# Kernel tuning notes

Hardware: AMD Instinct MI355X
Metric: run time of the kernel (lower is better)

Reference implementation:

```python
import jax, jax.numpy as jnp
import numpy as np

B, C_IN, N = 16, 64, 40962          # icosphere level-6 node count
C_OUT = 32                           # out_feats; conv emits 7*C_OUT channels
NEW_N = 4 * N - 6                    # 163842
SEVEN_N = 7 * N                      # gather domain after reshape


def setup_inputs() -> dict:
    key = jax.random.key(0)
    k1, k2, k3, k4, k5 = jax.random.split(key, 5)
    x = jax.random.normal(k1, (B, C_IN, N), dtype=jnp.float32)
    W = jax.random.normal(k2, (7 * C_OUT, C_IN), dtype=jnp.float32) * (1.0 / np.sqrt(C_IN))
    b = jax.random.normal(k3, (7 * C_OUT,), dtype=jnp.float32) * 0.01
    top_idx = jax.random.randint(k4, (N,), 0, SEVEN_N, dtype=jnp.int64 if jax.config.jax_enable_x64 else jnp.int32)
    down_idx = jax.random.randint(k5, ((3 * N - 6) * 2,), 0, SEVEN_N, dtype=jnp.int64 if jax.config.jax_enable_x64 else jnp.int32)
    return {"x": x, "W": W, "b": b, "top_idx": top_idx, "down_idx": down_idx}


def reference(x, W, b, top_idx, down_idx):
    Bsz, _, n = x.shape
    c_out = W.shape[0] // 7
    # pointwise (kernel_size=1) Conv1d == GEMM over channels: [B,7*out,N]
    y = jnp.einsum('bcn,oc->bon', x, W) + b[None, :, None]
    # torch .view(B, out, 7N): row-major reshape, identical in jax
    y = y.reshape(Bsz, c_out, 7 * n)
    x1 = y[:, :, top_idx]                               # [B, out, N]
    x2 = y[:, :, down_idx].reshape(Bsz, c_out, -1, 2)   # [B, out, 3N-6, 2]
    out = jnp.concatenate([x1, x2.mean(axis=3)], axis=2)  # [B, out, 4N-6]
    return out
```

## Files before the change

### kernel.cpp

```cpp
#include <hip/hip_runtime.h>
#include <hip/hip_fp16.h>

#define BB     16
#define CIN    64
#define NN     40962
#define COUT   32
#define NEWN   (4*NN - 6)
#define GROUPS_PER_B ((NEWN + 31)/32)
#define NGROUPS (BB * GROUPS_PER_B)

typedef _Float16 f16x8  __attribute__((ext_vector_type(8)));
typedef float    f32x16 __attribute__((ext_vector_type(16)));
typedef _Float16 h2     __attribute__((ext_vector_type(2)));

__device__ __forceinline__ int pk_add_h2(int a, int b) {
  h2 r = __builtin_bit_cast(h2, a) + __builtin_bit_cast(h2, b);
  return __builtin_bit_cast(int, r);
}
__device__ __forceinline__ int pack2(float lo, float hi) {
  h2 r; r.x = (_Float16)lo; r.y = (_Float16)hi;
  return __builtin_bit_cast(int, r);
}

__global__ __launch_bounds__(256) void k_transpose(const float* __restrict__ x,
                                                   __half* __restrict__ xT) {
  __shared__ float tile[64][65];
  const int b  = blockIdx.y;
  const int n0 = blockIdx.x * 64;
  const int lx = threadIdx.x & 63;
  const int ly = threadIdx.x >> 6;
  const float* xb = x + (size_t)b * CIN * NN;
  const int n = n0 + lx;
#pragma unroll
  for (int i = 0; i < 16; ++i) {
    int c = i * 4 + ly;
    tile[c][lx] = (n < NN) ? xb[(size_t)c * NN + n] : 0.f;
  }
  __syncthreads();
  __half* xTb = xT + (size_t)b * NN * CIN;
#pragma unroll
  for (int i = 0; i < 16; ++i) {
    int nl = i * 4 + ly;
    int nn = n0 + nl;
    if (nn < NN) xTb[(size_t)nn * CIN + lx] = __float2half(tile[lx][nl]);
  }
}

__global__ __launch_bounds__(256, 2) void k_upconv_mfma(
    const __half* __restrict__ xT, const float* __restrict__ W,
    const float* __restrict__ bias, const int* __restrict__ top,
    const int* __restrict__ down, float* __restrict__ out) {
  const int lane = threadIdx.x & 63;
  const int co   = lane & 31;
  const int h    = lane >> 5;
  const int waveInBlock = threadIdx.x >> 6;
  const int gwave = blockIdx.x * (blockDim.x >> 6) + waveInBlock;
  const int nwaves = gridDim.x * (blockDim.x >> 6);

  int4 Af[29];
#pragma unroll
  for (int s = 0; s < 28; ++s) {
    const int t  = s >> 2;
    const int c0 = 16 * (s & 3) + 8 * h;
    const float* wr = W + (co * 7 + t) * 64 + c0;
    float4 wa = *(const float4*)wr;
    float4 wb = *(const float4*)(wr + 4);
    Af[s].x = pack2(0.5f * wa.x, 0.5f * wa.y);
    Af[s].y = pack2(0.5f * wa.z, 0.5f * wa.w);
    Af[s].z = pack2(0.5f * wb.x, 0.5f * wb.y);
    Af[s].w = pack2(0.5f * wb.z, 0.5f * wb.w);
  }
  {
    int4 ab = {0, 0, 0, 0};
    if (h == 0) {
      float bv[8];
#pragma unroll
      for (int tau = 0; tau < 7; ++tau) bv[tau] = 0.5f * bias[co * 7 + tau];
      bv[7] = 0.f;
      ab.x = pack2(bv[0], bv[1]);
      ab.y = pack2(bv[2], bv[3]);
      ab.z = pack2(bv[4], bv[5]);
      ab.w = pack2(bv[6], bv[7]);
    }
    Af[28] = ab;
  }

  for (int gid = gwave; gid < NGROUPS; gid += nwaves) {
    const int b = gid / GROUPS_PER_B;
    const int g = gid - b * GROUPS_PER_B;
    const int k = g * 32 + co;
    const bool valid = (k < NEWN);

    int j1 = 0, j2 = 0;
    if (valid) {
      if (k < NN) { j1 = top[k]; j2 = j1; }
      else {
        const int kk = k - NN;
        j1 = down[2 * kk];
        j2 = down[2 * kk + 1];
      }
    }
    const int t0 = j1 / NN, n0 = j1 - t0 * NN;
    const int t1 = j2 / NN, n1 = j2 - t1 * NN;

    const __half* xTb = xT + (size_t)b * NN * CIN;
    const int4* base0 = (const int4*)(xTb + (size_t)n0 * CIN);
    const int4* base1 = (const int4*)(xTb + (size_t)n1 * CIN);
    int4 col0[4], col1[4];
#pragma unroll
    for (int q = 0; q < 4; ++q) col0[q] = base0[2 * q + h];
#pragma unroll
    for (int q = 0; q < 4; ++q) col1[q] = base1[2 * q + h];

    f32x16 acc;
#pragma unroll
    for (int i = 0; i < 16; ++i) acc[i] = 0.f;

#pragma unroll
    for (int s = 0; s < 28; ++s) {
      const int t = s >> 2, q = s & 3;
      const bool m0 = (t0 == t), m1 = (t1 == t);
      int4 bb;
      bb.x = pk_add_h2(m0 ? col0[q].x : 0, m1 ? col1[q].x : 0);
      bb.y = pk_add_h2(m0 ? col0[q].y : 0, m1 ? col1[q].y : 0);
      bb.z = pk_add_h2(m0 ? col0[q].z : 0, m1 ? col1[q].z : 0);
      bb.w = pk_add_h2(m0 ? col0[q].w : 0, m1 ? col1[q].w : 0);
      acc = __builtin_amdgcn_mfma_f32_32x32x16_f16(
          __builtin_bit_cast(f16x8, Af[s]), __builtin_bit_cast(f16x8, bb), acc, 0, 0, 0);
    }

    {
      int4 bsel = {0, 0, 0, 0};
      if (h == 0) {
        float c0f = (float)((t0 == 0) + (t1 == 0));
        float c1f = (float)((t0 == 1) + (t1 == 1));
        float c2f = (float)((t0 == 2) + (t1 == 2));
        float c3f = (float)((t0 == 3) + (t1 == 3));
        float c4f = (float)((t0 == 4) + (t1 == 4));
        float c5f = (float)((t0 == 5) + (t1 == 5));
        float c6f = (float)((t0 == 6) + (t1 == 6));
        bsel.x = pack2(c0f, c1f);
        bsel.y = pack2(c2f, c3f);
        bsel.z = pack2(c4f, c5f);
        bsel.w = pack2(c6f, 0.f);
      }
      acc = __builtin_amdgcn_mfma_f32_32x32x16_f16(
          __builtin_bit_cast(f16x8, Af[28]), __builtin_bit_cast(f16x8, bsel), acc, 0, 0, 0);
    }

    if (valid) {
      float* ob = out + (size_t)b * COUT * NEWN + k;
#pragma unroll
      for (int r = 0; r < 16; ++r) {
        const int corow = (r & 3) + 8 * (r >> 2) + 4 * h;
        ob[(size_t)corow * NEWN] = acc[r];
      }
    }
  }
}

#define WPB 68
#define TPB (32*WPB + 4)

__global__ __launch_bounds__(256) void k_upconv_f32(
    const float* __restrict__ x, const float* __restrict__ W,
    const float* __restrict__ bias, const int* __restrict__ top,
    const int* __restrict__ down, float* __restrict__ out) {
  __shared__ float wl[7 * TPB];
  __shared__ float bl[224];
  const int tid = threadIdx.x;
  for (int p = tid; p < 224 * 64; p += 256) {
    int o = p >> 6, c = p & 63;
    wl[(o % 7) * TPB + (o / 7) * WPB + c] = W[p];
  }
  if (tid < 224) bl[tid] = bias[tid];
  __syncthreads();

  const int b = blockIdx.y;
  const int k = blockIdx.x * 256 + tid;

  int nit = 0, t0 = 0, t1 = 0, n0 = 0, n1 = 0;
  if (k < NEWN) {
    if (k < NN) {
      int j = top[k];
      t0 = j / NN; n0 = j - t0 * NN; nit = 1;
    } else {
      int kk = k - NN;
      int j1 = down[2 * kk], j2 = down[2 * kk + 1];
      t0 = j1 / NN; n0 = j1 - t0 * NN;
      t1 = j2 / NN; n1 = j2 - t1 * NN;
      nit = 2;
    }
  }

  float acc[32];
#pragma unroll
  for (int i = 0; i < 32; ++i) acc[i] = 0.f;

  for (int it = 0; it < nit; ++it) {
    const int t = it ? t1 : t0;
    const int n = it ? n1 : n0;
    const float* col = x + (size_t)b * CIN * NN + n;
    const int base = t * TPB;
#pragma unroll
    for (int ch = 0; ch < 8; ++ch) {
      float xv[8];
#pragma unroll
      for (int q = 0; q < 8; ++q) xv[q] = col[(size_t)(ch * 8 + q) * NN];
#pragma unroll
      for (int co = 0; co < 32; ++co) {
        float a = acc[co];
        const float* wr = &wl[base + co * WPB + ch * 8];
        float4 w0 = *(const float4*)(wr);
        float4 w1 = *(const float4*)(wr + 4);
        a += w0.x * xv[0]; a += w0.y * xv[1]; a += w0.z * xv[2]; a += w0.w * xv[3];
        a += w1.x * xv[4]; a += w1.y * xv[5]; a += w1.z * xv[6]; a += w1.w * xv[7];
        acc[co] = a;
      }
    }
  }

  if (k < NEWN) {
    float* ob = out + (size_t)b * COUT * NEWN + k;
    if (k < NN) {
#pragma unroll
      for (int co = 0; co < 32; ++co)
        ob[(size_t)co * NEWN] = acc[co] + bl[co * 7 + t0];
    } else {
#pragma unroll
      for (int co = 0; co < 32; ++co)
        ob[(size_t)co * NEWN] = 0.5f * (acc[co] + bl[co * 7 + t0] + bl[co * 7 + t1]);
    }
  }
}

extern "C" void kernel_launch(void* const* d_in, const int* in_sizes, int n_in,
                              void* d_out, int out_size, void* d_ws, size_t ws_size,
                              hipStream_t stream) {
  const float* x    = (const float*)d_in[0];
  const float* W    = (const float*)d_in[1];
  const float* bias = (const float*)d_in[2];
  const int*   top  = (const int*)d_in[3];
  const int*   down = (const int*)d_in[4];
  float* out = (float*)d_out;

  const size_t xT_bytes = (size_t)BB * NN * CIN * sizeof(__half);
  if (ws_size >= xT_bytes) {
    __half* xT = (__half*)d_ws;
    k_transpose<<<dim3((NN + 63) / 64, BB), 256, 0, stream>>>(x, xT);
    k_upconv_mfma<<<dim3(512), 256, 0, stream>>>(xT, W, bias, top, down, out);
  } else {
    k_upconv_f32<<<dim3((NEWN + 255) / 256, BB), 256, 0, stream>>>(x, W, bias, top, down, out);
  }
}
```

Before: 614.7 us.

## Software-pipeline gather loads in MFMA kernel and vectorize transpose accesses

The main kernel loop is restructured into a two-stage software pipeline that issues the index and xT gather loads for the next group before computing and storing the current one, to hide gather latency. Output stores switch to nontemporal. The transpose kernel now reads float2 and writes packed 16-byte half vectors instead of scalar halves. Carrying a second group's prefetched registers raises register pressure, which may reduce occupancy.

```diff
diff --git a/kernel.cpp b/kernel.cpp
--- a/kernel.cpp
+++ b/kernel.cpp
@@ -25,24 +25,127 @@
 __global__ __launch_bounds__(256) void k_transpose(const float* __restrict__ x,
                                                    __half* __restrict__ xT) {
   __shared__ float tile[64][65];
-  const int b  = blockIdx.y;
-  const int n0 = blockIdx.x * 64;
-  const int lx = threadIdx.x & 63;
-  const int ly = threadIdx.x >> 6;
+  const int b   = blockIdx.y;
+  const int n0  = blockIdx.x * 64;
+  const int tid = threadIdx.x;
   const float* xb = x + (size_t)b * CIN * NN;
-  const int n = n0 + lx;
-#pragma unroll
-  for (int i = 0; i < 16; ++i) {
-    int c = i * 4 + ly;
-    tile[c][lx] = (n < NN) ? xb[(size_t)c * NN + n] : 0.f;
+
+  const int cr8 = tid >> 5;
+  const int nh  = tid & 31;
+  if (n0 + 64 <= NN) {
+#pragma unroll
+    for (int p = 0; p < 8; ++p) {
+      const int c = p * 8 + cr8;
+      float2 v = *reinterpret_cast<const float2*>(xb + (size_t)c * NN + n0 + nh * 2);
+      tile[c][nh * 2 + 0] = v.x;
+      tile[c][nh * 2 + 1] = v.y;
+    }
+  } else {
+#pragma unroll
+    for (int p = 0; p < 8; ++p) {
+      const int c = p * 8 + cr8;
+      const int na = n0 + nh * 2, nb = na + 1;
+      tile[c][nh * 2 + 0] = (na < NN) ? xb[(size_t)c * NN + na] : 0.f;
+      tile[c][nh * 2 + 1] = (nb < NN) ? xb[(size_t)c * NN + nb] : 0.f;
+    }
   }
   __syncthreads();
+
   __half* xTb = xT + (size_t)b * NN * CIN;
-#pragma unroll
-  for (int i = 0; i < 16; ++i) {
-    int nl = i * 4 + ly;
-    int nn = n0 + nl;
-    if (nn < NN) xTb[(size_t)nn * CIN + lx] = __float2half(tile[lx][nl]);
+  const int nr = tid >> 3;
+  const int ch = tid & 7;
+#pragma unroll
+  for (int p = 0; p < 2; ++p) {
+    const int nl = p * 32 + nr;
+    const int n  = n0 + nl;
+    if (n < NN) {
+      int4 v;
+      v.x = pack2(tile[ch * 8 + 0][nl], tile[ch * 8 + 1][nl]);
+      v.y = pack2(tile[ch * 8 + 2][nl], tile[ch * 8 + 3][nl]);
+      v.z = pack2(tile[ch * 8 + 4][nl], tile[ch * 8 + 5][nl]);
+      v.w = pack2(tile[ch * 8 + 6][nl], tile[ch * 8 + 7][nl]);
+      *reinterpret_cast<int4*>(xTb + (size_t)n * CIN + ch * 8) = v;
+    }
+  }
+}
+
+struct GD {
+  int4 c0[4], c1[4];
+  int  t0, t1;
+  int  b, k;
+  bool valid;
+};
+
+__device__ __forceinline__ GD load_group(int gid, const __half* __restrict__ xT,
+                                         const int* __restrict__ top,
+                                         const int* __restrict__ down,
+                                         int co, int h) {
+  GD d;
+  const int b = gid / GROUPS_PER_B;
+  const int g = gid - b * GROUPS_PER_B;
+  const int k = g * 32 + co;
+  d.b = b; d.k = k;
+  d.valid = (k < NEWN);
+  int j1 = 0, j2 = 0;
+  if (d.valid) {
+    if (k < NN) { j1 = top[k]; j2 = j1; }
+    else {
+      int2 jj = *reinterpret_cast<const int2*>(down + 2 * (k - NN));
+      j1 = jj.x; j2 = jj.y;
+    }
+  }
+  const int t0 = j1 / NN, n0 = j1 - t0 * NN;
+  const int t1 = j2 / NN, n1 = j2 - t1 * NN;
+  d.t0 = t0; d.t1 = t1;
+  const __half* xTb = xT + (size_t)b * NN * CIN;
+  const int4* b0 = (const int4*)(xTb + (size_t)n0 * CIN);
+  const int4* b1 = (const int4*)(xTb + (size_t)n1 * CIN);
+#pragma unroll
+  for (int q = 0; q < 4; ++q) d.c0[q] = b0[2 * q + h];
+#pragma unroll
+  for (int q = 0; q < 4; ++q) d.c1[q] = b1[2 * q + h];
+  return d;
+}
+
+__device__ __forceinline__ void compute_store(const GD& d, const int4* __restrict__ Af,
+                                              float* __restrict__ out, int h) {
+  f32x16 acc;
+#pragma unroll
+  for (int i = 0; i < 16; ++i) acc[i] = 0.f;
+  const int t0 = d.t0, t1 = d.t1;
+
+#pragma unroll
+  for (int s = 0; s < 28; ++s) {
+    const int t = s >> 2, q = s & 3;
+    const bool m0 = (t0 == t), m1 = (t1 == t);
+    int4 bb;
+    bb.x = pk_add_h2(m0 ? d.c0[q].x : 0, m1 ? d.c1[q].x : 0);
+    bb.y = pk_add_h2(m0 ? d.c0[q].y : 0, m1 ? d.c1[q].y : 0);
+    bb.z = pk_add_h2(m0 ? d.c0[q].z : 0, m1 ? d.c1[q].z : 0);
+    bb.w = pk_add_h2(m0 ? d.c0[q].w : 0, m1 ? d.c1[q].w : 0);
+    acc = __builtin_amdgcn_mfma_f32_32x32x16_f16(
+        __builtin_bit_cast(f16x8, Af[s]), __builtin_bit_cast(f16x8, bb), acc, 0, 0, 0);
+  }
+
+  {
+    int4 bsel = {0, 0, 0, 0};
+    if (h == 0) {
+      bsel.x = pack2((float)((t0 == 0) + (t1 == 0)), (float)((t0 == 1) + (t1 == 1)));
+      bsel.y = pack2((float)((t0 == 2) + (t1 == 2)), (float)((t0 == 3) + (t1 == 3)));
+      bsel.z = pack2((float)((t0 == 4) + (t1 == 4)), (float)((t0 == 5) + (t1 == 5)));
+      bsel.w = pack2((float)((t0 == 6) + (t1 == 6)), 0.f);
+    }
+    acc = __builtin_amdgcn_mfma_f32_32x32x16_f16(
+        __builtin_bit_cast(f16x8, Af[28]), __builtin_bit_cast(f16x8, bsel), acc, 0, 0, 0);
+  }
+
+  if (d.valid) {
+    float* ob = out + (size_t)d.b * COUT * NEWN + d.k;
+#pragma unroll
+    for (int r = 0; r < 16; ++r) {
+      const int corow = (r & 3) + 8 * (r >> 2) + 4 * h;
+      __builtin_nontemporal_store(acc[r], ob + (size_t)corow * NEWN);
+    }
   }
 }
 
@@ -53,8 +156,7 @@
   const int lane = threadIdx.x & 63;
   const int co   = lane & 31;
   const int h    = lane >> 5;
-  const int waveInBlock = threadIdx.x >> 6;
-  const int gwave = blockIdx.x * (blockDim.x >> 6) + waveInBlock;
+  const int gwave  = blockIdx.x * (blockDim.x >> 6) + (threadIdx.x >> 6);
   const int nwaves = gridDim.x * (blockDim.x >> 6);
 
   int4 Af[29];
@@ -85,77 +187,22 @@
     Af[28] = ab;
   }
 
-  for (int gid = gwave; gid < NGROUPS; gid += nwaves) {
-    const int b = gid / GROUPS_PER_B;
-    const int g = gid - b * GROUPS_PER_B;
-    const int k = g * 32 + co;
-    const bool valid = (k < NEWN);
-
-    int j1 = 0, j2 = 0;
-    if (valid) {
-      if (k < NN) { j1 = top[k]; j2 = j1; }
-      else {
-        const int kk = k - NN;
-        j1 = down[2 * kk];
-        j2 = down[2 * kk + 1];
-      }
-    }
-    const int t0 = j1 / NN, n0 = j1 - t0 * NN;
-    const int t1 = j2 / NN, n1 = j2 - t1 * NN;
-
-    const __half* xTb = xT + (size_t)b * NN * CIN;
-    const int4* base0 = (const int4*)(xTb + (size_t)n0 * CIN);
-    const int4* base1 = (const int4*)(xTb + (size_t)n1 * CIN);
-    int4 col0[4], col1[4];
-#pragma unroll
-    for (int q = 0; q < 4; ++q) col0[q] = base0[2 * q + h];
-#pragma unroll
-    for (int q = 0; q < 4; ++q) col1[q] = base1[2 * q + h];
-
-    f32x16 acc;
-#pragma unroll
-    for (int i = 0; i < 16; ++i) acc[i] = 0.f;
-
-#pragma unroll
-    for (int s = 0; s < 28; ++s) {
-      const int t = s >> 2, q = s & 3;
-      const bool m0 = (t0 == t), m1 = (t1 == t);
-      int4 bb;
-      bb.x = pk_add_h2(m0 ? col0[q].x : 0, m1 ? col1[q].x : 0);
-      bb.y = pk_add_h2(m0 ? col0[q].y : 0, m1 ? col1[q].y : 0);
-      bb.z = pk_add_h2(m0 ? col0[q].z : 0, m1 ? col1[q].z : 0);
-      bb.w = pk_add_h2(m0 ? col0[q].w : 0, m1 ? col1[q].w : 0);
-      acc = __builtin_amdgcn_mfma_f32_32x32x16_f16(
-          __builtin_bit_cast(f16x8, Af[s]), __builtin_bit_cast(f16x8, bb), acc, 0, 0, 0);
-    }
-
-    {
-      int4 bsel = {0, 0, 0, 0};
-      if (h == 0) {
-        float c0f = (float)((t0 == 0) + (t1 == 0));
-        float c1f = (float)((t0 == 1) + (t1 == 1));
-        float c2f = (float)((t0 == 2) + (t1 == 2));
-        float c3f = (float)((t0 == 3) + (t1 == 3));
-        float c4f = (float)((t0 == 4) + (t1 == 4));
-        float c5f = (float)((t0 == 5) + (t1 == 5));
-        float c6f = (float)((t0 == 6) + (t1 == 6));
-        bsel.x = pack2(c0f, c1f);
-        bsel.y = pack2(c2f, c3f);
-        bsel.z = pack2(c4f, c5f);
-        bsel.w = pack2(c6f, 0.f);
-      }
-      acc = __builtin_amdgcn_mfma_f32_32x32x16_f16(
-          __builtin_bit_cast(f16x8, Af[28]), __builtin_bit_cast(f16x8, bsel), acc, 0, 0, 0);
-    }
-
-    if (valid) {
-      float* ob = out + (size_t)b * COUT * NEWN + k;
-#pragma unroll
-      for (int r = 0; r < 16; ++r) {
-        const int corow = (r & 3) + 8 * (r >> 2) + 4 * h;
-        ob[(size_t)corow * NEWN] = acc[r];
-      }
-    }
+  int gid = gwave;
+  GD a = load_group(gid, xT, top, down, co, h);
+  for (;;) {
+    const int g1 = gid + nwaves;
+    const bool h1 = (g1 < NGROUPS);
+    GD bN;
+    if (h1) bN = load_group(g1, xT, top, down, co, h);
+    compute_store(a, Af, out, h);
+    if (!h1) return;
+
+    const int g2 = g1 + nwaves;
+    const bool h2 = (g2 < NGROUPS);
+    if (h2) a = load_group(g2, xT, top, down, co, h);
+    compute_store(bN, Af, out, h);
+    if (!h2) return;
+    gid = g2;
   }
 }
 
```

New measurement: 673.4 us. +9.5%, slower.
